# Optimization experiments

Hardware: AMD Instinct MI355X
Metric: run time of the kernel (lower is better)

The kernel has to match this reference:

```python
import jax, jax.numpy as jnp
import numpy as np

B, L, H, Z, T = 128, 4096, 1024, 256, 16  # batch, input_len(64*64), lstm_hidden, z_size, timesteps


def _lstm_cell(x, h, c, W_ih, b_ih, W_hh, b_hh):
    # PyTorch LSTMCell: gates ordered (input, forget, cell, output)
    gates = x @ W_ih.T + b_ih + h @ W_hh.T + b_hh
    i, f, g, o = jnp.split(gates, 4, axis=-1)
    c_new = jax.nn.sigmoid(f) * c + jax.nn.sigmoid(i) * jnp.tanh(g)
    h_new = jax.nn.sigmoid(o) * jnp.tanh(c_new)
    return h_new, c_new


def setup_inputs() -> dict:
    key = jax.random.key(0)
    ks = jax.random.split(key, 16)
    s = 0.02  # weight init scale
    return {
        "x": jax.random.uniform(ks[0], (B, L), dtype=jnp.float32),
        "eps": jax.random.normal(ks[1], (T, B, Z), dtype=jnp.float32),
        "c_0": jax.random.normal(ks[2], (1, L), dtype=jnp.float32),
        "h_0_enc": jax.random.normal(ks[3], (H,), dtype=jnp.float32),
        "h_0_dec": jax.random.normal(ks[4], (H,), dtype=jnp.float32),
        "W_ih_enc": jax.random.normal(ks[5], (4 * H, 2 * L + H), dtype=jnp.float32) * s,
        "b_ih_enc": jnp.zeros((4 * H,), dtype=jnp.float32),
        "W_hh_enc": jax.random.normal(ks[6], (4 * H, H), dtype=jnp.float32) * s,
        "b_hh_enc": jnp.zeros((4 * H,), dtype=jnp.float32),
        "W_mu": jax.random.normal(ks[7], (Z, H), dtype=jnp.float32) * s,
        "b_mu": jnp.zeros((Z,), dtype=jnp.float32),
        "W_sigma": jax.random.normal(ks[8], (Z, H), dtype=jnp.float32) * s,
        "b_sigma": jnp.zeros((Z,), dtype=jnp.float32),
        "W_ih_dec": jax.random.normal(ks[9], (4 * H, Z), dtype=jnp.float32) * s,
        "b_ih_dec": jnp.zeros((4 * H,), dtype=jnp.float32),
        "W_hh_dec": jax.random.normal(ks[10], (4 * H, H), dtype=jnp.float32) * s,
        "b_hh_dec": jnp.zeros((4 * H,), dtype=jnp.float32),
        "W_write": jax.random.normal(ks[11], (L, H), dtype=jnp.float32) * s,
        "b_write": jnp.zeros((L,), dtype=jnp.float32),
    }


def reference(x, eps, c_0, h_0_enc, h_0_dec,
              W_ih_enc, b_ih_enc, W_hh_enc, b_hh_enc,
              W_mu, b_mu, W_sigma, b_sigma,
              W_ih_dec, b_ih_dec, W_hh_dec, b_hh_dec,
              W_write, b_write):
    batch = x.shape[0]
    c_t = jnp.broadcast_to(c_0, (batch, L))
    h_enc = jnp.broadcast_to(h_0_enc, (batch, H))
    h_dec = jnp.broadcast_to(h_0_dec, (batch, H))
    c_enc = jnp.zeros((batch, H), dtype=x.dtype)
    c_dec = jnp.zeros((batch, H), dtype=x.dtype)

    def step(carry, eps_t):
        c_t, h_enc, c_enc, h_dec, c_dec = carry
        x_hat = x - jax.nn.sigmoid(c_t)
        r_t = jnp.concatenate((x, x_hat, h_dec), axis=-1)  # read + concat with h_dec
        h_enc, c_enc = _lstm_cell(r_t, h_enc, c_enc, W_ih_enc, b_ih_enc, W_hh_enc, b_hh_enc)
        mu = h_enc @ W_mu.T + b_mu
        logsigma = h_enc @ W_sigma.T + b_sigma
        z_t = eps_t * jnp.exp(logsigma) + mu
        h_dec, c_dec = _lstm_cell(z_t, h_dec, c_dec, W_ih_dec, b_ih_dec, W_hh_dec, b_hh_dec)
        c_t = c_t + h_dec @ W_write.T + b_write
        return (c_t, h_enc, c_enc, h_dec, c_dec), None

    (c_t, _, _, _, _), _ = jax.lax.scan(step, (c_t, h_enc, c_enc, h_dec, c_dec), eps)
    return jax.nn.sigmoid(c_t)
```

## Files before the change

kernel.cpp:

```cpp
#include <hip/hip_runtime.h>

#define B_   128
#define T_   16

typedef __bf16 bf16;
typedef __bf16 bf16x4 __attribute__((ext_vector_type(4)));
typedef __bf16 bf16x8 __attribute__((ext_vector_type(8)));
typedef float f32x4 __attribute__((ext_vector_type(4)));

#define GLL(SRC, DST) __builtin_amdgcn_global_load_lds( \
    (const __attribute__((address_space(1))) void*)(SRC), \
    (__attribute__((address_space(3))) void*)(DST), 16, 0, 0)

#define MFMA __builtin_amdgcn_mfma_f32_16x16x32_bf16
#define SLICE 524288

__device__ __forceinline__ float sigf(float x) { return 1.f / (1.f + expf(-x)); }

__device__ __forceinline__ void core64(
    bf16 (&As)[2][4096], bf16 (&Bs)[2][4096],
    const bf16* __restrict__ Ab, int lda,
    const bf16* __restrict__ Wb, int ldw,
    int nk, f32x4 (&acc)[4])
{
    const int tid = threadIdx.x, lane = tid & 63, wave = tid >> 6;
    const int srow = lane >> 3;
    const int scol = ((lane & 7) ^ srow) << 3;
    const int wr = wave & 1, wc = wave >> 1;
    const int ln = lane & 15;
    const int rA0 = wr * 32 + ln;
    const int rB0 = wc * 32 + ln;
    const int swz = (lane & 7) << 4;
    const int kq  = (lane >> 4) << 4;

    auto stage = [&](int b, int koff) {
        int c0 = wave, c1 = wave + 4;
        int ra0 = c0 * 8 + srow, ra1 = c1 * 8 + srow;
        GLL(Ab + (size_t)ra0 * lda + koff + scol, &As[b][c0 * 512]);
        GLL(Ab + (size_t)ra1 * lda + koff + scol, &As[b][c1 * 512]);
        GLL(Wb + (size_t)ra0 * ldw + koff + scol, &Bs[b][c0 * 512]);
        GLL(Wb + (size_t)ra1 * ldw + koff + scol, &Bs[b][c1 * 512]);
    };

    stage(0, 0);
    int bq = 0;
    for (int it = 0; it < nk; ++it) {
        __syncthreads();
        if (it + 1 < nk) stage(bq ^ 1, (it + 1) << 6);
        const bf16* as = As[bq];
        const bf16* bs = Bs[bq];
#pragma unroll
        for (int k2 = 0; k2 < 2; ++k2) {
            const int co = (((k2 << 6) | kq) ^ swz) >> 1;
            bf16x8 a0 = *(const bf16x8*)&as[rA0 * 64 + co];
            bf16x8 a1 = *(const bf16x8*)&as[(rA0 + 16) * 64 + co];
            bf16x8 b0 = *(const bf16x8*)&bs[rB0 * 64 + co];
            bf16x8 b1 = *(const bf16x8*)&bs[(rB0 + 16) * 64 + co];
            acc[0] = MFMA(a0, b0, acc[0], 0, 0, 0);
            acc[1] = MFMA(a0, b1, acc[1], 0, 0, 0);
            acc[2] = MFMA(a1, b0, acc[2], 0, 0, 0);
            acc[3] = MFMA(a1, b1, acc[3], 0, 0, 0);
        }
        bq ^= 1;
    }
}

__device__ __forceinline__ void store64f(float* __restrict__ P, int bm, int bn,
                                         f32x4 (&acc)[4])
{
    const int lane = threadIdx.x & 63, wave = threadIdx.x >> 6;
    const int wr = wave & 1, wc = wave >> 1;
    const int ln = lane & 15, q = lane >> 4;
    const int row0 = bm + wr * 32 + q * 4;
    const int col0 = bn + wc * 32 + ln;
#pragma unroll
    for (int r = 0; r < 4; ++r) {
        P[(size_t)(row0 + r) * 4096 + col0]           = acc[0][r];
        P[(size_t)(row0 + r) * 4096 + col0 + 16]      = acc[1][r];
        P[(size_t)(row0 + 16 + r) * 4096 + col0]      = acc[2][r];
        P[(size_t)(row0 + 16 + r) * 4096 + col0 + 16] = acc[3][r];
    }
}

__device__ __forceinline__ void store64b(bf16* __restrict__ P, int bm, int bn,
                                         f32x4 (&acc)[4])
{
    const int lane = threadIdx.x & 63, wave = threadIdx.x >> 6;
    const int wr = wave & 1, wc = wave >> 1;
    const int ln = lane & 15, q = lane >> 4;
    const int row0 = bm + wr * 32 + q * 4;
    const int col0 = bn + wc * 32 + ln;
#pragma unroll
    for (int r = 0; r < 4; ++r) {
        P[(size_t)(row0 + r) * 4096 + col0]           = (bf16)acc[0][r];
        P[(size_t)(row0 + r) * 4096 + col0 + 16]      = (bf16)acc[1][r];
        P[(size_t)(row0 + 16 + r) * 4096 + col0]      = (bf16)acc[2][r];
        P[(size_t)(row0 + 16 + r) * 4096 + col0 + 16] = (bf16)acc[3][r];
    }
}

__global__ __launch_bounds__(256) void gemm64_k(
    const bf16* __restrict__ A, int lda,
    const bf16* __restrict__ W, int ldw, int Kc,
    float* __restrict__ P)
{
    __shared__ bf16 As[2][4096], Bs[2][4096];
    const int nt = blockIdx.x, mt = blockIdx.y, zz = blockIdx.z;
    f32x4 acc[4];
#pragma unroll
    for (int i = 0; i < 4; ++i) acc[i] = (f32x4){0.f, 0.f, 0.f, 0.f};
    const bf16* Ab = A + (size_t)mt * 64 * lda + (size_t)zz * Kc;
    const bf16* Wb = W + (size_t)nt * 64 * ldw + (size_t)zz * Kc;
    core64(As, Bs, Ab, lda, Wb, ldw, Kc >> 6, acc);
    store64f(P + (size_t)zz * SLICE, mt * 64, nt * 64, acc);
}

__global__ __launch_bounds__(256) void kAE_k(
    const bf16* __restrict__ negs, const bf16* __restrict__ hh,
    const bf16* __restrict__ Wxh,  const bf16* __restrict__ Wcat,
    const bf16* __restrict__ Wdh,
    bf16* __restrict__ encP, bf16* __restrict__ decP)
{
    __shared__ bf16 As[2][4096], Bs[2][4096];
    const int bid = blockIdx.x;
    const int swz = (bid & 7) * 224 + (bid >> 3);
    const int mt = swz & 1, nt = (swz >> 1) & 63, zz = swz >> 7;

    const bf16 *Ab, *Wb;
    int lda, ldw;
    bf16* P;
    if (zz < 8) {
        Ab = negs + (size_t)mt * 64 * 4096 + zz * 512; lda = 4096;
        Wb = Wxh  + (size_t)nt * 64 * 4096 + zz * 512; ldw = 4096;
        P = encP + (size_t)zz * SLICE;
    } else if (zz < 12) {
        int s = zz - 8;
        Ab = hh   + (size_t)mt * 64 * 2048 + s * 512;  lda = 2048;
        Wb = Wcat + (size_t)nt * 64 * 2048 + s * 512;  ldw = 2048;
        P = encP + (size_t)(8 + s) * SLICE;
    } else {
        int g = zz - 12;
        Ab = hh  + (size_t)mt * 64 * 2048 + g * 512;   lda = 2048;
        Wb = Wdh + (size_t)nt * 64 * 1024 + g * 512;   ldw = 1024;
        P = decP + (size_t)g * SLICE;
    }
    f32x4 acc[4];
#pragma unroll
    for (int i = 0; i < 4; ++i) acc[i] = (f32x4){0.f, 0.f, 0.f, 0.f};
    core64(As, Bs, Ab, lda, Wb, ldw, 8, acc);
    store64b(P, mt * 64, nt * 64, acc);
}

__global__ __launch_bounds__(256) void kW_k(
    const bf16* __restrict__ hh, const bf16* __restrict__ Wwr,
    bf16* __restrict__ wrP)
{
    __shared__ bf16 As[2][4096], Bs[2][4096];
    const int bid = blockIdx.x;
    const int swz = (bid & 7) * 32 + (bid >> 3);
    const int mt = swz & 1, nt = (swz >> 1) & 63, zz = swz >> 7;
    const bf16* Ab = hh  + (size_t)mt * 64 * 2048 + zz * 512;
    const bf16* Wb = Wwr + (size_t)nt * 64 * 1024 + zz * 512;
    f32x4 acc[4];
#pragma unroll
    for (int i = 0; i < 4; ++i) acc[i] = (f32x4){0.f, 0.f, 0.f, 0.f};
    core64(As, Bs, Ab, 2048, Wb, 1024, 8, acc);
    store64b(wrP + (size_t)zz * SLICE, mt * 64, nt * 64, acc);
}

__global__ __launch_bounds__(256) void fin0_k(
    const float* __restrict__ P, float* __restrict__ base,
    const float* __restrict__ b1, const float* __restrict__ b2)
{
    const int i = blockIdx.x * 256 + threadIdx.x;
    const int row = i >> 10, j = i & 1023;
    const size_t off = (size_t)row * 4096 + (j << 2);
    float s0 = 0.f, s1 = 0.f, s2 = 0.f, s3 = 0.f;
#pragma unroll
    for (int z = 0; z < 4; ++z) {
        float4 p = *(const float4*)(P + (size_t)z * SLICE + off);
        s0 += p.x; s1 += p.y; s2 += p.z; s3 += p.w;
    }
    base[off + 0] = s0 + b1[j]        + b2[j];
    base[off + 1] = s1 + b1[1024 + j] + b2[1024 + j];
    base[off + 2] = s2 + b1[2048 + j] + b2[2048 + j];
    base[off + 3] = s3 + b1[3072 + j] + b2[3072 + j];
}

__global__ __launch_bounds__(256) void kB_k(
    const bf16* __restrict__ encP, const float* __restrict__ base,
    float* __restrict__ c_enc, bf16* __restrict__ hh)
{
    const int i = blockIdx.x * 256 + threadIdx.x;
    const int row = i >> 10, j = i & 1023;
    const size_t off = (size_t)row * 4096 + (j << 2);
    float s0 = 0.f, s1 = 0.f, s2 = 0.f, s3 = 0.f;
#pragma unroll
    for (int z = 0; z < 12; ++z) {
        bf16x4 p = *(const bf16x4*)(encP + (size_t)z * SLICE + off);
        s0 += (float)p[0]; s1 += (float)p[1]; s2 += (float)p[2]; s3 += (float)p[3];
    }
    float4 bb = *(const float4*)(base + off);
    float gi = s0 + bb.x, gf = s1 + bb.y, gg = s2 + bb.z, go = s3 + bb.w;
    float cn = sigf(gf) * c_enc[i] + sigf(gi) * tanhf(gg);
    c_enc[i] = cn;
    hh[(size_t)row * 2048 + 1024 + j] = (bf16)(sigf(go) * tanhf(cn));
}

__global__ __launch_bounds__(256) void kF_k(
    const bf16* __restrict__ wrP, const float* __restrict__ b_wr,
    float* __restrict__ c_t, bf16* __restrict__ negs, float* __restrict__ outp)
{
    const int qi = blockIdx.x * 256 + threadIdx.x;
    const int row = qi >> 10, cq = qi & 1023;
    const size_t off = (size_t)row * 4096 + (cq << 2);
    bf16x4 p0 = *(const bf16x4*)(wrP + off);
    bf16x4 p1 = *(const bf16x4*)(wrP + SLICE + off);
    float4 cv = *(const float4*)(c_t + off);
    float4 bw = *(const float4*)(b_wr + (cq << 2));
    float v0 = cv.x + (float)p0[0] + (float)p1[0] + bw.x;
    float v1 = cv.y + (float)p0[1] + (float)p1[1] + bw.y;
    float v2 = cv.z + (float)p0[2] + (float)p1[2] + bw.z;
    float v3 = cv.w + (float)p0[3] + (float)p1[3] + bw.w;
    *(float4*)(c_t + off) = make_float4(v0, v1, v2, v3);
    negs[off + 0] = (bf16)(-sigf(v0));
    negs[off + 1] = (bf16)(-sigf(v1));
    negs[off + 2] = (bf16)(-sigf(v2));
    negs[off + 3] = (bf16)(-sigf(v3));
    if (outp)
        *(float4*)(outp + off) = make_float4(sigf(v0), sigf(v1), sigf(v2), sigf(v3));
}

struct SmemG32 {
    bf16 As[4][128][64];
    bf16 Ws[4][32][64];
};

__global__ __launch_bounds__(256) void kC_k(
    const bf16* __restrict__ hh, const bf16* __restrict__ Wms,
    const float* __restrict__ b_mu, const float* __restrict__ b_sig,
    const float* __restrict__ eps_t, bf16* __restrict__ zbf)
{
    __shared__ SmemG32 sm;
    const int nt = blockIdx.x;
    const int tid = threadIdx.x, lane = tid & 63, wave = tid >> 6;
    const int srow = lane >> 3, scol = ((lane & 7) ^ srow) << 3;
    const int ln = lane & 15, kq = (lane >> 4) << 4;
    const int swz = (lane & 7) << 4;
    const int rA = wave * 32 + ln;
    const bf16* Wb = Wms + (size_t)nt * 32 * 1024;
    const bf16* Ab = hh + 1024;

    f32x4 acc[2][2];
#pragma unroll
    for (int m = 0; m < 2; ++m)
#pragma unroll
        for (int n = 0; n < 2; ++n) acc[m][n] = (f32x4){0.f, 0.f, 0.f, 0.f};

    for (int it = 0; it < 4; ++it) {
        if (it) __syncthreads();
        const int koff = it * 256;
#pragma unroll
        for (int kc = 0; kc < 4; ++kc) {
            const int kg = koff + kc * 64 + scol;
#pragma unroll
            for (int i = 0; i < 4; ++i) {
                int rb = i * 32 + wave * 8;
                GLL(Ab + (size_t)(rb + srow) * 2048 + kg, &sm.As[kc][rb][0]);
            }
            GLL(Wb + (size_t)(wave * 8 + srow) * 1024 + kg, &sm.Ws[kc][wave * 8][0]);
        }
        __syncthreads();
#pragma unroll
        for (int kc = 0; kc < 4; ++kc)
#pragma unroll
            for (int k2 = 0; k2 < 2; ++k2) {
                const int co = (((k2 << 6) | kq) ^ swz) >> 1;
                bf16x8 a0 = *(const bf16x8*)&sm.As[kc][rA][co];
                bf16x8 a1 = *(const bf16x8*)&sm.As[kc][rA + 16][co];
                bf16x8 b0 = *(const bf16x8*)&sm.Ws[kc][ln][co];
                bf16x8 b1 = *(const bf16x8*)&sm.Ws[kc][ln + 16][co];
                acc[0][0] = MFMA(a0, b0, acc[0][0], 0, 0, 0);
                acc[0][1] = MFMA(a0, b1, acc[0][1], 0, 0, 0);
                acc[1][0] = MFMA(a1, b0, acc[1][0], 0, 0, 0);
                acc[1][1] = MFMA(a1, b1, acc[1][1], 0, 0, 0);
            }
    }
    __syncthreads();

    float* Cl = (float*)&sm;
    const int q = lane >> 4;
#pragma unroll
    for (int f = 0; f < 2; ++f)
#pragma unroll
        for (int n = 0; n < 2; ++n)
#pragma unroll
            for (int r = 0; r < 4; ++r)
                Cl[(wave * 32 + f * 16 + q * 4 + r) * 33 + n * 16 + ln] = acc[f][n][r];
    __syncthreads();

#pragma unroll
    for (int it = 0; it < 8; ++it) {
        int li = it * 256 + tid;
        int row = li >> 4, zl = li & 15;
        int zi = nt * 16 + zl;
        float mu = Cl[row * 33 + zl * 2]     + b_mu[zi];
        float ls = Cl[row * 33 + zl * 2 + 1] + b_sig[zi];
        float z = eps_t[row * 256 + zi] * expf(ls) + mu;
        zbf[(size_t)row * 256 + zi] = (bf16)z;
    }
}

struct SmemK { bf16 A[2][4096]; bf16 B[2][4096]; };

__global__ __launch_bounds__(256) void kD_k(
    const bf16* __restrict__ zbf, const bf16* __restrict__ Wdz,
    const bf16* __restrict__ decP,
    const float* __restrict__ b_ihd, const float* __restrict__ b_hhd,
    float* __restrict__ c_dec, bf16* __restrict__ hh)
{
    __shared__ SmemK sm;
    const int bid = blockIdx.x;
    const int mt = bid & 1, nt = bid >> 1;
    const int tid = threadIdx.x, lane = tid & 63, wave = tid >> 6;
    const int wr = wave & 1, wc = wave >> 1;
    const int ln = lane & 15, q = lane >> 4;

    const bf16* Ab = zbf + (size_t)mt * 64 * 256;
    const bf16* Wb = Wdz + (size_t)nt * 64 * 256;
    f32x4 acc[4];
#pragma unroll
    for (int i = 0; i < 4; ++i) acc[i] = (f32x4){0.f, 0.f, 0.f, 0.f};
    core64(sm.A, sm.B, Ab, 256, Wb, 256, 4, acc);

    __syncthreads();
    float* Cl = (float*)&sm;
    const int r0 = wr * 32 + q * 4;
    const int c0 = wc * 32 + ln;
#pragma unroll
    for (int r = 0; r < 4; ++r) {
        Cl[(r0 + r) * 66 + c0]           = acc[0][r];
        Cl[(r0 + r) * 66 + c0 + 16]      = acc[1][r];
        Cl[(r0 + 16 + r) * 66 + c0]      = acc[2][r];
        Cl[(r0 + 16 + r) * 66 + c0 + 16] = acc[3][r];
    }
    __syncthreads();

#pragma unroll
    for (int it = 0; it < 4; ++it) {
        int li = it * 256 + tid;
        int lrow = li >> 4, jl = li & 15;
        int row = mt * 64 + lrow;
        int np0 = nt * 64 + jl * 4;
        int J = np0 >> 2;
        const float* cr = &Cl[lrow * 66 + jl * 4];
        const bf16* gp = decP + (size_t)row * 4096 + np0;
        bf16x4 g0v = *(const bf16x4*)gp;
        bf16x4 g1v = *(const bf16x4*)(gp + SLICE);
        float gi = cr[0] + (float)g0v[0] + (float)g1v[0] + b_ihd[J]        + b_hhd[J];
        float gf = cr[1] + (float)g0v[1] + (float)g1v[1] + b_ihd[1024 + J] + b_hhd[1024 + J];
        float gg = cr[2] + (float)g0v[2] + (float)g1v[2] + b_ihd[2048 + J] + b_hhd[2048 + J];
        float go = cr[3] + (float)g0v[3] + (float)g1v[3] + b_ihd[3072 + J] + b_hhd[3072 + J];
        int ci = row * 1024 + J;
        float cn = sigf(gf) * c_dec[ci] + sigf(gi) * tanhf(gg);
        c_dec[ci] = cn;
        hh[(size_t)row * 2048 + J] = (bf16)(sigf(go) * tanhf(cn));
    }
}

#define PBL (B_ * 4096)
#define PBH (B_ * 1024)

__global__ void init_k(const float* __restrict__ x, const float* __restrict__ c0,
                       const float* __restrict__ h0e, const float* __restrict__ h0d,
                       float* __restrict__ c_t, float* __restrict__ c_enc,
                       float* __restrict__ c_dec, bf16* __restrict__ negs,
                       bf16* __restrict__ hh, bf16* __restrict__ x_bf) {
    int i = blockIdx.x * 256 + threadIdx.x;
    if (i >= PBL) return;
    int n = i & 4095;
    float c = c0[n];
    c_t[i] = c;
    negs[i] = (bf16)(-sigf(c));
    x_bf[i] = (bf16)x[i];
    if (i < PBH) {
        int row = i >> 10, j = i & 1023;
        c_enc[i] = 0.f;
        c_dec[i] = 0.f;
        hh[(size_t)row * 2048 + j]        = (bf16)h0d[j];
        hh[(size_t)row * 2048 + 1024 + j] = (bf16)h0e[j];
    }
}

__device__ __forceinline__ bf16x8 cvt8(const float* s) {
    float4 a = *(const float4*)s, b = *(const float4*)(s + 4);
    bf16x8 v = { (bf16)a.x, (bf16)a.y, (bf16)a.z, (bf16)a.w,
                 (bf16)b.x, (bf16)b.y, (bf16)b.z, (bf16)b.w };
    return v;
}

__global__ void conv_es_k(const float* __restrict__ Wih, const float* __restrict__ Whh,
                          bf16* __restrict__ wxh, bf16* __restrict__ wsum,
                          bf16* __restrict__ wcat) {
    int id = blockIdx.x * 256 + threadIdx.x;
    if (id >= 4096 * 768) return;
    int np = id / 768, c = (id - np * 768) * 8;
    int n = ((np & 3) << 10) + (np >> 2);
    if (c < 4096) {
        const float* sx = Wih + (size_t)n * 9216 + c;
        const float* sh = sx + 4096;
        float4 a = *(const float4*)sh, b = *(const float4*)(sh + 4);
        float4 e = *(const float4*)sx, f = *(const float4*)(sx + 4);
        bf16x8 vh = { (bf16)a.x, (bf16)a.y, (bf16)a.z, (bf16)a.w,
                      (bf16)b.x, (bf16)b.y, (bf16)b.z, (bf16)b.w };
        bf16x8 vs = { (bf16)(a.x + e.x), (bf16)(a.y + e.y), (bf16)(a.z + e.z), (bf16)(a.w + e.w),
                      (bf16)(b.x + f.x), (bf16)(b.y + f.y), (bf16)(b.z + f.z), (bf16)(b.w + f.w) };
        *(bf16x8*)(wxh  + (size_t)np * 4096 + c) = vh;
        *(bf16x8*)(wsum + (size_t)np * 4096 + c) = vs;
    } else if (c < 5120) {
        *(bf16x8*)(wcat + (size_t)np * 2048 + (c - 4096)) =
            cvt8(Wih + (size_t)n * 9216 + 8192 + (c - 4096));
    } else {
        *(bf16x8*)(wcat + (size_t)np * 2048 + 1024 + (c - 5120)) =
            cvt8(Whh + (size_t)n * 1024 + (c - 5120));
    }
}

__global__ void conv_dec_k(const float* __restrict__ Wih, const float* __restrict__ Whh,
                           bf16* __restrict__ wdz, bf16* __restrict__ wdh) {
    int id = blockIdx.x * 256 + threadIdx.x;
    if (id >= 4096 * 160) return;
    int np = id / 160, c = (id - np * 160) * 8;
    int n = ((np & 3) << 10) + (np >> 2);
    if (c < 256)
        *(bf16x8*)(wdz + (size_t)np * 256 + c) = cvt8(Wih + (size_t)n * 256 + c);
    else
        *(bf16x8*)(wdh + (size_t)np * 1024 + (c - 256)) =
            cvt8(Whh + (size_t)n * 1024 + (c - 256));
}

__global__ void conv_ms_k(const float* __restrict__ Wmu, const float* __restrict__ Wsig,
                          bf16* __restrict__ dst) {
    int id = blockIdx.x * 256 + threadIdx.x;
    if (id >= 512 * 128) return;
    int np = id >> 7, c = (id & 127) * 8;
    int zi = np >> 1;
    const float* src = ((np & 1) ? Wsig : Wmu) + (size_t)zi * 1024 + c;
    *(bf16x8*)(dst + (size_t)np * 1024 + c) = cvt8(src);
}

__global__ void conv_wr_k(const float* __restrict__ Wwr, bf16* __restrict__ dst) {
    int id = blockIdx.x * 256 + threadIdx.x;
    if (id >= 4096 * 128) return;
    *(bf16x8*)(dst + (size_t)id * 8) = cvt8(Wwr + (size_t)id * 8);
}

extern "C" void kernel_launch(void* const* d_in, const int* in_sizes, int n_in,
                              void* d_out, int out_size, void* d_ws, size_t ws_size,
                              hipStream_t stream) {
    const float* x      = (const float*)d_in[0];
    const float* eps    = (const float*)d_in[1];
    const float* c0     = (const float*)d_in[2];
    const float* h0e    = (const float*)d_in[3];
    const float* h0d    = (const float*)d_in[4];
    const float* W_ih_e = (const float*)d_in[5];
    const float* b_ih_e = (const float*)d_in[6];
    const float* W_hh_e = (const float*)d_in[7];
    const float* b_hh_e = (const float*)d_in[8];
    const float* W_mu   = (const float*)d_in[9];
    const float* b_mu   = (const float*)d_in[10];
    const float* W_sig  = (const float*)d_in[11];
    const float* b_sig  = (const float*)d_in[12];
    const float* W_ih_d = (const float*)d_in[13];
    const float* b_ih_d = (const float*)d_in[14];
    const float* W_hh_d = (const float*)d_in[15];
    const float* b_hh_d = (const float*)d_in[16];
    const float* W_wr   = (const float*)d_in[17];
    const float* b_wr   = (const float*)d_in[18];
    float* out = (float*)d_out;

    float* f = (float*)d_ws;
    float* c_t   = f; f += SLICE;
    float* base  = f; f += SLICE;
    float* pP    = f; f += (size_t)4 * SLICE;
    float* c_enc = f; f += 131072;
    float* c_dec = f; f += 131072;
    bf16* bp    = (bf16*)f;
    bf16* encP  = bp; bp += (size_t)12 * SLICE;
    bf16* decP  = bp; bp += (size_t)2 * SLICE;
    bf16* wrP   = bp; bp += (size_t)2 * SLICE;
    bf16* negs  = bp; bp += (size_t)B_ * 4096;
    bf16* hh    = bp; bp += (size_t)B_ * 2048;
    bf16* zbf   = bp; bp += (size_t)B_ * 256;
    bf16* x_bf  = bp; bp += (size_t)B_ * 4096;
    bf16* Wxh   = bp; bp += (size_t)4096 * 4096;
    bf16* Wsum  = bp; bp += (size_t)4096 * 4096;
    bf16* Wcat  = bp; bp += (size_t)4096 * 2048;
    bf16* Wdz   = bp; bp += (size_t)4096 * 256;
    bf16* Wdh   = bp; bp += (size_t)4096 * 1024;
    bf16* Wms   = bp; bp += (size_t)512 * 1024;
    bf16* Wwr   = bp; bp += (size_t)4096 * 1024;

    dim3 blk(256);

    init_k<<<(PBL + 255) / 256, blk, 0, stream>>>(x, c0, h0e, h0d, c_t, c_enc, c_dec,
                                                  negs, hh, x_bf);
    conv_es_k<<<(4096 * 768 + 255) / 256, blk, 0, stream>>>(W_ih_e, W_hh_e,
                                                            Wxh, Wsum, Wcat);
    conv_dec_k<<<(4096 * 160 + 255) / 256, blk, 0, stream>>>(W_ih_d, W_hh_d, Wdz, Wdh);
    conv_ms_k<<<(512 * 128 + 255) / 256, blk, 0, stream>>>(W_mu, W_sig, Wms);
    conv_wr_k<<<(4096 * 128 + 255) / 256, blk, 0, stream>>>(W_wr, Wwr);

    gemm64_k<<<dim3(64, 2, 4), blk, 0, stream>>>(x_bf, 4096, Wsum, 4096, 1024, pP);
    fin0_k<<<dim3(512), blk, 0, stream>>>(pP, base, b_ih_e, b_hh_e);

    kAE_k<<<dim3(1792), blk, 0, stream>>>(negs, hh, Wxh, Wcat, Wdh, encP, decP);

    for (int t = 0; t < T_; ++t) {
        kB_k<<<dim3(512), blk, 0, stream>>>(encP, base, c_enc, hh);
        kC_k<<<dim3(16), blk, 0, stream>>>(hh, Wms, b_mu, b_sig,
                                           eps + (size_t)t * (B_ * 256), zbf);
        kD_k<<<dim3(128), blk, 0, stream>>>(zbf, Wdz, decP, b_ih_d, b_hh_d, c_dec, hh);
        kW_k<<<dim3(256), blk, 0, stream>>>(hh, Wwr, wrP);
        kF_k<<<dim3(512), blk, 0, stream>>>(wrP, b_wr, c_t, negs,
                                            (t == T_ - 1) ? out : nullptr);
        if (t < T_ - 1)
            kAE_k<<<dim3(1792), blk, 0, stream>>>(negs, hh, Wxh, Wcat, Wdh, encP, decP);
    }
}
```

Baseline: 863.0 us.

## Fuse write GEMM with c_t epilogue and reorder per-step kernel schedule

The write-projection GEMM now runs with full K in one block and applies the c_t update, sigmoid and negs/output writes directly in its epilogue, removing the split-K partial buffer and the separate kF elementwise kernel. The Wcat and Wdh GEMMs that depend only on hh are merged into the same launch, so they overlap with the write GEMM. The negs-dependent Wxh GEMM moves to the start of the next step as its own launch. This cuts one launch and a round trip through global memory per step. In exchange the write GEMM has fewer, longer blocks with no K-split, and the negs GEMM now sits on the critical path alone.

```diff
diff --git a/kernel.cpp b/kernel.cpp
--- a/kernel.cpp
+++ b/kernel.cpp
@@ -115,57 +115,84 @@
     store64f(P + (size_t)zz * SLICE, mt * 64, nt * 64, acc);
 }
 
-__global__ __launch_bounds__(256) void kAE_k(
-    const bf16* __restrict__ negs, const bf16* __restrict__ hh,
-    const bf16* __restrict__ Wxh,  const bf16* __restrict__ Wcat,
-    const bf16* __restrict__ Wdh,
-    bf16* __restrict__ encP, bf16* __restrict__ decP)
+__global__ __launch_bounds__(256) void gemm64b_k(
+    const bf16* __restrict__ A, int lda,
+    const bf16* __restrict__ W, int ldw, int Kc,
+    bf16* __restrict__ P)
 {
     __shared__ bf16 As[2][4096], Bs[2][4096];
-    const int bid = blockIdx.x;
-    const int swz = (bid & 7) * 224 + (bid >> 3);
-    const int mt = swz & 1, nt = (swz >> 1) & 63, zz = swz >> 7;
-
-    const bf16 *Ab, *Wb;
-    int lda, ldw;
-    bf16* P;
-    if (zz < 8) {
-        Ab = negs + (size_t)mt * 64 * 4096 + zz * 512; lda = 4096;
-        Wb = Wxh  + (size_t)nt * 64 * 4096 + zz * 512; ldw = 4096;
-        P = encP + (size_t)zz * SLICE;
-    } else if (zz < 12) {
-        int s = zz - 8;
-        Ab = hh   + (size_t)mt * 64 * 2048 + s * 512;  lda = 2048;
-        Wb = Wcat + (size_t)nt * 64 * 2048 + s * 512;  ldw = 2048;
-        P = encP + (size_t)(8 + s) * SLICE;
-    } else {
-        int g = zz - 12;
-        Ab = hh  + (size_t)mt * 64 * 2048 + g * 512;   lda = 2048;
-        Wb = Wdh + (size_t)nt * 64 * 1024 + g * 512;   ldw = 1024;
-        P = decP + (size_t)g * SLICE;
-    }
+    const int nt = blockIdx.x, mt = blockIdx.y, zz = blockIdx.z;
     f32x4 acc[4];
 #pragma unroll
     for (int i = 0; i < 4; ++i) acc[i] = (f32x4){0.f, 0.f, 0.f, 0.f};
-    core64(As, Bs, Ab, lda, Wb, ldw, 8, acc);
-    store64b(P, mt * 64, nt * 64, acc);
-}
-
-__global__ __launch_bounds__(256) void kW_k(
-    const bf16* __restrict__ hh, const bf16* __restrict__ Wwr,
-    bf16* __restrict__ wrP)
+    const bf16* Ab = A + (size_t)mt * 64 * lda + (size_t)zz * Kc;
+    const bf16* Wb = W + (size_t)nt * 64 * ldw + (size_t)zz * Kc;
+    core64(As, Bs, Ab, lda, Wb, ldw, Kc >> 6, acc);
+    store64b(P + (size_t)zz * SLICE, mt * 64, nt * 64, acc);
+}
+
+__global__ __launch_bounds__(256) void kE2_k(
+    const bf16* __restrict__ hh,   const bf16* __restrict__ Wwr,
+    const bf16* __restrict__ Wcat, const bf16* __restrict__ Wdh,
+    float* __restrict__ c_t, bf16* __restrict__ negs,
+    const float* __restrict__ b_wr,
+    bf16* __restrict__ encP, bf16* __restrict__ decP,
+    float* __restrict__ outp, int bid_off)
 {
     __shared__ bf16 As[2][4096], Bs[2][4096];
-    const int bid = blockIdx.x;
-    const int swz = (bid & 7) * 32 + (bid >> 3);
-    const int mt = swz & 1, nt = (swz >> 1) & 63, zz = swz >> 7;
+    const int bid = blockIdx.x + bid_off;
+    f32x4 acc[4];
+#pragma unroll
+    for (int i = 0; i < 4; ++i) acc[i] = (f32x4){0.f, 0.f, 0.f, 0.f};
+
+    if (bid < 128) {
+        const int mt = bid & 1, nt = bid >> 1;
+        const bf16* Ab = hh  + (size_t)mt * 64 * 2048;
+        const bf16* Wb = Wwr + (size_t)nt * 64 * 1024;
+        core64(As, Bs, Ab, 2048, Wb, 1024, 16, acc);
+
+        const int lane = threadIdx.x & 63, wave = threadIdx.x >> 6;
+        const int wrw = wave & 1, wcw = wave >> 1;
+        const int ln = lane & 15, q = lane >> 4;
+        const int row0 = mt * 64 + wrw * 32 + q * 4;
+        const int col0 = nt * 64 + wcw * 32 + ln;
+#pragma unroll
+        for (int r = 0; r < 4; ++r) {
+#pragma unroll
+            for (int hb = 0; hb < 2; ++hb) {
+                int row = row0 + hb * 16 + r;
+#pragma unroll
+                for (int cb = 0; cb < 2; ++cb) {
+                    int col = col0 + cb * 16;
+                    float a = acc[hb * 2 + cb][r];
+                    size_t idx = (size_t)row * 4096 + col;
+                    float v = c_t[idx] + a + b_wr[col];
+                    c_t[idx] = v;
+                    float sv = sigf(v);
+                    negs[idx] = (bf16)(-sv);
+                    if (outp) outp[idx] = sv;
+                }
+            }
+        }
+        return;
+    }
+
+    if (bid < 640) {
+        const int r = bid - 128;
+        const int zz = r & 3, mt = (r >> 2) & 1, nt = r >> 3;
+        const bf16* Ab = hh   + (size_t)mt * 64 * 2048 + zz * 512;
+        const bf16* Wb = Wcat + (size_t)nt * 64 * 2048 + zz * 512;
+        core64(As, Bs, Ab, 2048, Wb, 2048, 8, acc);
+        store64b(encP + (size_t)(8 + zz) * SLICE, mt * 64, nt * 64, acc);
+        return;
+    }
+
+    const int r = bid - 640;
+    const int zz = r & 1, mt = (r >> 1) & 1, nt = r >> 2;
     const bf16* Ab = hh  + (size_t)mt * 64 * 2048 + zz * 512;
-    const bf16* Wb = Wwr + (size_t)nt * 64 * 1024 + zz * 512;
-    f32x4 acc[4];
-#pragma unroll
-    for (int i = 0; i < 4; ++i) acc[i] = (f32x4){0.f, 0.f, 0.f, 0.f};
+    const bf16* Wb = Wdh + (size_t)nt * 64 * 1024 + zz * 512;
     core64(As, Bs, Ab, 2048, Wb, 1024, 8, acc);
-    store64b(wrP + (size_t)zz * SLICE, mt * 64, nt * 64, acc);
+    store64b(decP + (size_t)zz * SLICE, mt * 64, nt * 64, acc);
 }
 
 __global__ __launch_bounds__(256) void fin0_k(
@@ -205,30 +232,6 @@
     float cn = sigf(gf) * c_enc[i] + sigf(gi) * tanhf(gg);
     c_enc[i] = cn;
     hh[(size_t)row * 2048 + 1024 + j] = (bf16)(sigf(go) * tanhf(cn));
-}
-
-__global__ __launch_bounds__(256) void kF_k(
-    const bf16* __restrict__ wrP, const float* __restrict__ b_wr,
-    float* __restrict__ c_t, bf16* __restrict__ negs, float* __restrict__ outp)
-{
-    const int qi = blockIdx.x * 256 + threadIdx.x;
-    const int row = qi >> 10, cq = qi & 1023;
-    const size_t off = (size_t)row * 4096 + (cq << 2);
-    bf16x4 p0 = *(const bf16x4*)(wrP + off);
-    bf16x4 p1 = *(const bf16x4*)(wrP + SLICE + off);
-    float4 cv = *(const float4*)(c_t + off);
-    float4 bw = *(const float4*)(b_wr + (cq << 2));
-    float v0 = cv.x + (float)p0[0] + (float)p1[0] + bw.x;
-    float v1 = cv.y + (float)p0[1] + (float)p1[1] + bw.y;
-    float v2 = cv.z + (float)p0[2] + (float)p1[2] + bw.z;
-    float v3 = cv.w + (float)p0[3] + (float)p1[3] + bw.w;
-    *(float4*)(c_t + off) = make_float4(v0, v1, v2, v3);
-    negs[off + 0] = (bf16)(-sigf(v0));
-    negs[off + 1] = (bf16)(-sigf(v1));
-    negs[off + 2] = (bf16)(-sigf(v2));
-    negs[off + 3] = (bf16)(-sigf(v3));
-    if (outp)
-        *(float4*)(outp + off) = make_float4(sigf(v0), sigf(v1), sigf(v2), sigf(v3));
 }
 
 struct SmemG32 {
@@ -488,7 +491,6 @@
     bf16* bp    = (bf16*)f;
     bf16* encP  = bp; bp += (size_t)12 * SLICE;
     bf16* decP  = bp; bp += (size_t)2 * SLICE;
-    bf16* wrP   = bp; bp += (size_t)2 * SLICE;
     bf16* negs  = bp; bp += (size_t)B_ * 4096;
     bf16* hh    = bp; bp += (size_t)B_ * 2048;
     bf16* zbf   = bp; bp += (size_t)B_ * 256;
@@ -514,17 +516,20 @@
     gemm64_k<<<dim3(64, 2, 4), blk, 0, stream>>>(x_bf, 4096, Wsum, 4096, 1024, pP);
     fin0_k<<<dim3(512), blk, 0, stream>>>(pP, base, b_ih_e, b_hh_e);
 
-    kAE_k<<<dim3(1792), blk, 0, stream>>>(negs, hh, Wxh, Wcat, Wdh, encP, decP);
+    kE2_k<<<dim3(768), blk, 0, stream>>>(hh, Wwr, Wcat, Wdh, c_t, negs, b_wr,
+                                         encP, decP, nullptr, 128);
 
     for (int t = 0; t < T_; ++t) {
+        gemm64b_k<<<dim3(64, 2, 8), blk, 0, stream>>>(negs, 4096, Wxh, 4096, 512, encP);
         kB_k<<<dim3(512), blk, 0, stream>>>(encP, base, c_enc, hh);
         kC_k<<<dim3(16), blk, 0, stream>>>(hh, Wms, b_mu, b_sig,
                                            eps + (size_t)t * (B_ * 256), zbf);
         kD_k<<<dim3(128), blk, 0, stream>>>(zbf, Wdz, decP, b_ih_d, b_hh_d, c_dec, hh);
-        kW_k<<<dim3(256), blk, 0, stream>>>(hh, Wwr, wrP);
-        kF_k<<<dim3(512), blk, 0, stream>>>(wrP, b_wr, c_t, negs,
-                                            (t == T_ - 1) ? out : nullptr);
         if (t < T_ - 1)
-            kAE_k<<<dim3(1792), blk, 0, stream>>>(negs, hh, Wxh, Wcat, Wdh, encP, decP);
-    }
-}
+            kE2_k<<<dim3(896), blk, 0, stream>>>(hh, Wwr, Wcat, Wdh, c_t, negs, b_wr,
+                                                 encP, decP, nullptr, 0);
+        else
+            kE2_k<<<dim3(128), blk, 0, stream>>>(hh, Wwr, Wcat, Wdh, c_t, negs, b_wr,
+                                                 encP, decP, out, 0);
+    }
+}
```

Measured after the change: 926.9 us. +7.4%, slower.
